# Optimization experiments

Measured on AMD Instinct MI355X. Metric: run time of the kernel, lower is better.

The kernel has to match this reference:

```python
import jax, jax.numpy as jnp
import numpy as np

N_HEADS = 16
WINDOW = 256


def setup_inputs() -> dict:
    key = jax.random.key(0)
    ks = jax.random.split(key, 6)
    B, S, D = 2, 2048, 1024
    std = 0.02
    x = jax.random.normal(ks[0], (B, S, D), dtype=jnp.float32)
    wq = jax.random.normal(ks[1], (D, D), dtype=jnp.float32) * std
    wk = jax.random.normal(ks[2], (D, D), dtype=jnp.float32) * std
    wv = jax.random.normal(ks[3], (D, D), dtype=jnp.float32) * std
    wo = jax.random.normal(ks[4], (D, D), dtype=jnp.float32) * std
    bq = jnp.zeros((D,), jnp.float32)
    bk = jnp.zeros((D,), jnp.float32)
    bv = jnp.zeros((D,), jnp.float32)
    bo = jnp.zeros((D,), jnp.float32)
    return {"x": x, "wq": wq, "bq": bq, "wk": wk, "bk": bk,
            "wv": wv, "bv": bv, "wo": wo, "bo": bo}


def _sliding_window_bias(seq_len: int) -> jnp.ndarray:
    # allowed iff |i - j| <= WINDOW  ->  0.0, else -inf  (matches torch loop mask)
    i = jnp.arange(seq_len)[:, None]
    j = jnp.arange(seq_len)[None, :]
    allowed = jnp.abs(i - j) <= WINDOW
    return jnp.where(allowed, 0.0, -jnp.inf).astype(jnp.float32)


def reference(x, wq, bq, wk, bk, wv, bv, wo, bo):
    B, S, D = x.shape
    H = N_HEADS
    dh = D // H
    scale = dh ** -0.5
    # nn.Linear: y = x @ W^T + b
    q = (x @ wq.T + bq).reshape(B, S, H, dh).transpose(0, 2, 1, 3)  # [B,H,S,dh]
    k = (x @ wk.T + bk).reshape(B, S, H, dh).transpose(0, 2, 1, 3)
    v = (x @ wv.T + bv).reshape(B, S, H, dh).transpose(0, 2, 1, 3)
    scores = jnp.einsum('bhqd,bhkd->bhqk', q, k) * scale  # [B,H,S,S]
    scores = scores + _sliding_window_bias(S)[None, None]
    attn = jax.nn.softmax(scores, axis=-1)
    out = jnp.einsum('bhqk,bhkd->bhqd', attn, v)  # [B,H,S,dh]
    out = out.transpose(0, 2, 1, 3).reshape(B, S, D)
    return out @ wo.T + bo
```

## Files before the change

kernel.cpp:

```cpp
#include <hip/hip_runtime.h>
#include <stdint.h>

static constexpr int Ss = 2048;
static constexpr int Dd = 1024;
static constexpr int Hh = 16;
static constexpr int DH = 64;

typedef short bf16x8 __attribute__((ext_vector_type(8)));
typedef float f32x4 __attribute__((ext_vector_type(4)));

#define LOG2E 1.4426950408889634f

__device__ __forceinline__ uint16_t f2bf(float f) {
  uint32_t u = __builtin_bit_cast(uint32_t, f);
  u += 0x7fffu + ((u >> 16) & 1u);
  return (uint16_t)(u >> 16);
}
__device__ __forceinline__ float bf2f(uint16_t h) {
  uint32_t u = ((uint32_t)h) << 16;
  return __builtin_bit_cast(float, u);
}
__device__ __forceinline__ uint32_t cvtpk(float a, float b) {
  uint32_t r;
  asm("v_cvt_pk_bf16_f32 %0, %1, %2" : "=v"(r) : "v"(a), "v"(b));
  return r;
}

template <int CTRL>
__device__ __forceinline__ float dppf(float x) {
  return __builtin_bit_cast(float,
      __builtin_amdgcn_update_dpp(0, __builtin_bit_cast(int, x), CTRL, 0xF, 0xF, true));
}
__device__ __forceinline__ float rowsum16(float v) {
  v += dppf<0x128>(v);
  v += dppf<0x124>(v);
  v += dppf<0x122>(v);
  v += dppf<0x121>(v);
  return v;
}
__device__ __forceinline__ float fexp2(float x) { return __builtin_amdgcn_exp2f(x); }

#define GAS(p) ((const __attribute__((address_space(1))) uint32_t*)(p))
#define LAS(p) ((__attribute__((address_space(3))) uint32_t*)(p))

__global__ void cvt_all(const float* __restrict__ x,
                        const float* __restrict__ w0, const float* __restrict__ w1,
                        const float* __restrict__ w2, const float* __restrict__ w3,
                        uint16_t* __restrict__ xb,
                        uint16_t* __restrict__ o0, uint16_t* __restrict__ o1,
                        uint16_t* __restrict__ o2, uint16_t* __restrict__ o3) {
  int bid = blockIdx.x;
  const float* in;
  uint16_t* out;
  int i;
  if (bid < 4096) {
    in = x; out = xb; i = bid * 256 + threadIdx.x;
  } else {
    int b2 = bid - 4096;
    int t = b2 >> 10;
    in = (t == 0) ? w0 : (t == 1) ? w1 : (t == 2) ? w2 : w3;
    out = (t == 0) ? o0 : (t == 1) ? o1 : (t == 2) ? o2 : o3;
    i = (b2 & 1023) * 256 + threadIdx.x;
  }
  float4 v = reinterpret_cast<const float4*>(in)[i];
  ushort4 o;
  o.x = f2bf(v.x); o.y = f2bf(v.y); o.z = f2bf(v.z); o.w = f2bf(v.w);
  reinterpret_cast<ushort4*>(out)[i] = o;
}

__global__ __launch_bounds__(256, 2) void gemm_qkv(
    const uint16_t* __restrict__ A,
    const uint16_t* __restrict__ W0, const uint16_t* __restrict__ W1, const uint16_t* __restrict__ W2,
    const float* __restrict__ b0, const float* __restrict__ b1, const float* __restrict__ b2,
    uint16_t* __restrict__ O0, uint16_t* __restrict__ O1, uint16_t* __restrict__ O2) {
  constexpr int K = 1024;
  __shared__ __align__(16) uint8_t ldsA[128 * 128];
  __shared__ __align__(16) uint8_t ldsB[128 * 128];

  const int tid = threadIdx.x, w = tid >> 6, lane = tid & 63;
  const int q = lane & 15, g = lane >> 4;
  const int wm = w >> 1, wn = w & 1;
  const int bx = blockIdx.x, by = blockIdx.y, z = blockIdx.z;
  const uint16_t* Wp = (z == 0) ? W0 : (z == 1) ? W1 : W2;
  const float* bp = (z == 0) ? b0 : (z == 1) ? b1 : b2;
  uint16_t* Op = (z == 0) ? O0 : (z == 1) ? O1 : O2;

  f32x4 acc[4][4] = {};

  const int nkt = K >> 6;
  for (int kt = 0; kt < nkt; ++kt) {
    const int k0 = kt << 6;
    __syncthreads();
#pragma unroll
    for (int i = 0; i < 4; ++i) {
      int Lb = w * 4096 + i * 1024 + lane * 16;
      int row = Lb >> 7, cb = Lb & 127;
      int col = (cb ^ ((row & 7) << 4)) >> 1;
      const uint16_t* srcA = A + (size_t)(bx * 128 + row) * K + k0 + col;
      __builtin_amdgcn_global_load_lds(GAS(srcA), LAS(ldsA + w * 4096 + i * 1024), 16, 0, 0);
      const uint16_t* srcB = Wp + (size_t)(by * 128 + row) * K + k0 + col;
      __builtin_amdgcn_global_load_lds(GAS(srcB), LAS(ldsB + w * 4096 + i * 1024), 16, 0, 0);
    }
    __syncthreads();

    bf16x8 af[4][2], bfg[4][2];
#pragma unroll
    for (int mi = 0; mi < 4; ++mi)
#pragma unroll
      for (int s = 0; s < 2; ++s) {
        int row = wm * 64 + mi * 16 + q;
        int cb = (16 * g + 64 * s) ^ ((row & 7) << 4);
        af[mi][s] = *(const bf16x8*)(ldsA + row * 128 + cb);
      }
#pragma unroll
    for (int ni = 0; ni < 4; ++ni)
#pragma unroll
      for (int s = 0; s < 2; ++s) {
        int row = wn * 64 + ni * 16 + q;
        int cb = (16 * g + 64 * s) ^ ((row & 7) << 4);
        bfg[ni][s] = *(const bf16x8*)(ldsB + row * 128 + cb);
      }
#pragma unroll
    for (int mi = 0; mi < 4; ++mi)
#pragma unroll
      for (int ni = 0; ni < 4; ++ni) {
        acc[mi][ni] = __builtin_amdgcn_mfma_f32_16x16x32_bf16(af[mi][0], bfg[ni][0], acc[mi][ni], 0, 0, 0);
        acc[mi][ni] = __builtin_amdgcn_mfma_f32_16x16x32_bf16(af[mi][1], bfg[ni][1], acc[mi][ni], 0, 0, 0);
      }
  }

  float bias[4];
#pragma unroll
  for (int ni = 0; ni < 4; ++ni) bias[ni] = bp[by * 128 + wn * 64 + ni * 16 + q];
#pragma unroll
  for (int mi = 0; mi < 4; ++mi)
#pragma unroll
    for (int ni = 0; ni < 4; ++ni)
#pragma unroll
      for (int r = 0; r < 4; ++r) {
        int m = bx * 128 + wm * 64 + mi * 16 + 4 * g + r;
        int n = by * 128 + wn * 64 + ni * 16 + q;
        float v = acc[mi][ni][r] + bias[ni];
        int b = m >> 11, s = m & 2047, h = n >> 6, d = n & 63;
        Op[(((size_t)(b * Hh + h) * Ss + s) << 6) + d] = f2bf(v);
      }
}

__global__ __launch_bounds__(256, 2) void gemm_out(
    const uint16_t* __restrict__ A, const uint16_t* __restrict__ W,
    const float* __restrict__ bp, float* __restrict__ O, int M, int N, int K) {
  __shared__ __align__(16) uint8_t ldsA[2][128 * 128];
  __shared__ __align__(16) uint8_t ldsB[2][64 * 128];

  const int tid = threadIdx.x, w = tid >> 6, lane = tid & 63;
  const int q = lane & 15, g = lane >> 4;
  const int wm = w >> 1, wn = w & 1;
  const int bx = blockIdx.x, by = blockIdx.y;

  f32x4 acc[4][2] = {};

  const int Lb4 = lane * 16;
  auto stage = [&](int kt, int buf) {
    const int k0 = kt << 6;
#pragma unroll
    for (int i = 0; i < 4; ++i) {
      int Lb = w * 4096 + i * 1024 + Lb4;
      int row = Lb >> 7, cb = Lb & 127;
      const uint16_t* srcA = A + (size_t)(bx * 128 + row) * K + k0 + ((cb ^ ((row & 7) << 4)) >> 1);
      __builtin_amdgcn_global_load_lds(GAS(srcA), LAS(ldsA[buf] + w * 4096 + i * 1024), 16, 0, 0);
    }
#pragma unroll
    for (int i = 0; i < 2; ++i) {
      int Lb = w * 2048 + i * 1024 + Lb4;
      int row = Lb >> 7, cb = Lb & 127;
      const uint16_t* srcB = W + (size_t)(by * 64 + row) * K + k0 + ((cb ^ ((row & 7) << 4)) >> 1);
      __builtin_amdgcn_global_load_lds(GAS(srcB), LAS(ldsB[buf] + w * 2048 + i * 1024), 16, 0, 0);
    }
  };

  stage(0, 0);

  const int nkt = K >> 6;
  for (int kt = 0; kt < nkt; ++kt) {
    const int cur = kt & 1;
    asm volatile("s_waitcnt vmcnt(0)" ::: "memory");
    __builtin_amdgcn_sched_barrier(0);
    __builtin_amdgcn_s_barrier();
    __builtin_amdgcn_sched_barrier(0);
    if (kt + 1 < nkt) stage(kt + 1, cur ^ 1);

    bf16x8 af[4][2], bfg[2][2];
#pragma unroll
    for (int mi = 0; mi < 4; ++mi)
#pragma unroll
      for (int s = 0; s < 2; ++s) {
        int row = wm * 64 + mi * 16 + q;
        int cb = (16 * g + 64 * s) ^ ((row & 7) << 4);
        af[mi][s] = *(const bf16x8*)(ldsA[cur] + row * 128 + cb);
      }
#pragma unroll
    for (int ni = 0; ni < 2; ++ni)
#pragma unroll
      for (int s = 0; s < 2; ++s) {
        int row = wn * 32 + ni * 16 + q;
        int cb = (16 * g + 64 * s) ^ ((row & 7) << 4);
        bfg[ni][s] = *(const bf16x8*)(ldsB[cur] + row * 128 + cb);
      }
#pragma unroll
    for (int mi = 0; mi < 4; ++mi)
#pragma unroll
      for (int ni = 0; ni < 2; ++ni) {
        acc[mi][ni] = __builtin_amdgcn_mfma_f32_16x16x32_bf16(af[mi][0], bfg[ni][0], acc[mi][ni], 0, 0, 0);
        acc[mi][ni] = __builtin_amdgcn_mfma_f32_16x16x32_bf16(af[mi][1], bfg[ni][1], acc[mi][ni], 0, 0, 0);
      }
  }

  float bias[2];
#pragma unroll
  for (int ni = 0; ni < 2; ++ni) bias[ni] = bp[by * 64 + wn * 32 + ni * 16 + q];
#pragma unroll
  for (int mi = 0; mi < 4; ++mi)
#pragma unroll
    for (int ni = 0; ni < 2; ++ni)
#pragma unroll
      for (int r = 0; r < 4; ++r) {
        int m = bx * 128 + wm * 64 + mi * 16 + 4 * g + r;
        int n = by * 64 + wn * 32 + ni * 16 + q;
        O[(size_t)m * N + n] = acc[mi][ni][r] + bias[ni];
      }
}

__global__ __launch_bounds__(512, 4) void attn_swa(
    const uint16_t* __restrict__ Qg, const uint16_t* __restrict__ Kg,
    const uint16_t* __restrict__ Vg, uint16_t* __restrict__ Og) {
  __shared__ __align__(16) uint8_t ldsK[2][64 * 128];
  __shared__ __align__(16) uint8_t ldsVt[2][64 * 128];
  __shared__ __align__(16) uint8_t ldsP[8][2048];

  const int tid = threadIdx.x, w = tid >> 6, lane = tid & 63;
  const int q = lane & 15, g = lane >> 4;
  const int qb = blockIdx.x, bh = blockIdx.y;
  const size_t hbase = (size_t)bh * Ss * DH;
  const uint16_t* Qp = Qg + hbase;
  const uint16_t* Kp = Kg + hbase;
  const uint16_t* Vp = Vg + hbase;
  const int q0 = qb * 128;
  const int qw = q0 + w * 16;

  bf16x8 aq[2];
#pragma unroll
  for (int s = 0; s < 2; ++s) {
    bf16x8 t = *(const bf16x8*)(Qp + (size_t)(qw + q) * DH + s * 32 + g * 8);
#pragma unroll
    for (int j = 0; j < 8; ++j) {
      float f = bf2f((uint16_t)t[j]) * 0.125f;
      t[j] = (short)f2bf(f);
    }
    aq[s] = t;
  }

  f32x4 accO[4] = {};
  float lrun[4] = {0.f, 0.f, 0.f, 0.f};

  const int t0 = (q0 >= 256) ? (q0 - 256) : 0;
  const int t1 = (q0 + 384 <= Ss) ? (q0 + 384) : Ss;
  const int nt = (t1 - t0) >> 6;

  {
    int Lb = w * 1024 + lane * 16;
    int row = Lb >> 7, cb = Lb & 127;
    const uint16_t* srcK = Kp + (size_t)(t0 + row) * DH + ((cb ^ ((row & 7) << 4)) >> 1);
    __builtin_amdgcn_global_load_lds(GAS(srcK), LAS(ldsK[0] + w * 1024), 16, 0, 0);
  }
  bf16x8 v0 = *(const bf16x8*)(Vp + (size_t)(t0 + lane) * DH + w * 8);

  for (int t = 0; t < nt; ++t) {
    const int kb0 = t0 + (t << 6);
    const int cur = t & 1, nxt = cur ^ 1;

    asm volatile("s_waitcnt vmcnt(0)" ::: "memory");
    uint8_t* Vt = ldsVt[cur];
#pragma unroll
    for (int j = 0; j < 8; ++j) {
      int c = w * 8 + j;
      *(uint16_t*)(Vt + c * 128 + ((2 * lane) ^ (j << 4))) = (uint16_t)v0[j];
    }
    asm volatile("s_waitcnt lgkmcnt(0)" ::: "memory");
    __builtin_amdgcn_sched_barrier(0);
    __builtin_amdgcn_s_barrier();
    __builtin_amdgcn_sched_barrier(0);

    if (t + 1 < nt) {
      int Lb = w * 1024 + lane * 16;
      int row = Lb >> 7, cb = Lb & 127;
      const uint16_t* srcK = Kp + (size_t)(kb0 + 64 + row) * DH + ((cb ^ ((row & 7) << 4)) >> 1);
      __builtin_amdgcn_global_load_lds(GAS(srcK), LAS(ldsK[nxt] + w * 1024), 16, 0, 0);
      v0 = *(const bf16x8*)(Vp + (size_t)(kb0 + 64 + lane) * DH + w * 8);
    }

    const int dtile = kb0 - qw;
    if (dtile >= -319 && dtile <= 271) {
      const uint8_t* Kl = ldsK[cur];
      f32x4 sacc[4] = {};
      __builtin_amdgcn_s_setprio(1);
#pragma unroll
      for (int kb = 0; kb < 4; ++kb) {
        int row = kb * 16 + q;
#pragma unroll
        for (int s = 0; s < 2; ++s) {
          int cb = (16 * g + 64 * s) ^ ((row & 7) << 4);
          bf16x8 bk = *(const bf16x8*)(Kl + row * 128 + cb);
          sacc[kb] = __builtin_amdgcn_mfma_f32_16x16x32_bf16(aq[s], bk, sacc[kb], 0, 0, 0);
        }
      }
      __builtin_amdgcn_s_setprio(0);
      if (dtile < -192 || dtile > 192) {
#pragma unroll
        for (int kb = 0; kb < 4; ++kb) {
          int key = kb0 + kb * 16 + q;
#pragma unroll
          for (int r = 0; r < 4; ++r) {
            int qi = qw + 4 * g + r;
            int dd = qi - key;
            bool ok = (dd <= 256) && (dd >= -256);
            sacc[kb][r] = ok ? sacc[kb][r] : -1e30f;
          }
        }
      }
      uint8_t* Pl = ldsP[w];
#pragma unroll
      for (int r = 0; r < 4; ++r) {
        float p0 = fexp2(sacc[0][r] * LOG2E);
        float p1 = fexp2(sacc[1][r] * LOG2E);
        float p2 = fexp2(sacc[2][r] * LOG2E);
        float p3 = fexp2(sacc[3][r] * LOG2E);
        float rs = rowsum16((p0 + p1) + (p2 + p3));
        lrun[r] += rs;
        int prow = 4 * g + r;
        int sw = (prow & 7) << 4;
        uint8_t* Pr = Pl + prow * 128;
        uint32_t pk01 = cvtpk(p0, p1), pk23 = cvtpk(p2, p3);
        *(uint16_t*)(Pr + ((2 * q) ^ sw))      = (uint16_t)pk01;
        *(uint16_t*)(Pr + ((2 * q + 32) ^ sw)) = (uint16_t)(pk01 >> 16);
        *(uint16_t*)(Pr + ((2 * q + 64) ^ sw)) = (uint16_t)pk23;
        *(uint16_t*)(Pr + ((2 * q + 96) ^ sw)) = (uint16_t)(pk23 >> 16);
      }
      bf16x8 ap[2];
#pragma unroll
      for (int s = 0; s < 2; ++s) {
        int cb = (16 * g + 64 * s) ^ ((q & 7) << 4);
        ap[s] = *(const bf16x8*)(Pl + q * 128 + cb);
      }
      __builtin_amdgcn_s_setprio(1);
#pragma unroll
      for (int db = 0; db < 4; ++db) {
        int vr = db * 16 + q;
#pragma unroll
        for (int s = 0; s < 2; ++s) {
          int cb = (64 * s + 16 * g) ^ ((vr & 7) << 4);
          bf16x8 bvf = *(const bf16x8*)(ldsVt[cur] + vr * 128 + cb);
          accO[db] = __builtin_amdgcn_mfma_f32_16x16x32_bf16(ap[s], bvf, accO[db], 0, 0, 0);
        }
      }
      __builtin_amdgcn_s_setprio(0);
    }
  }

  const int b2 = bh >> 4, h = bh & 15;
#pragma unroll
  for (int r = 0; r < 4; ++r) {
    float inv = 1.0f / lrun[r];
    int qi = qw + 4 * g + r;
    size_t rowbase = ((size_t)(b2 * Ss + qi)) * Dd + h * DH;
#pragma unroll
    for (int db = 0; db < 4; ++db) {
      Og[rowbase + db * 16 + q] = f2bf(accO[db][r] * inv);
    }
  }
}

extern "C" void kernel_launch(void* const* d_in, const int* in_sizes, int n_in,
                              void* d_out, int out_size, void* d_ws, size_t ws_size,
                              hipStream_t stream) {
  const float* x  = (const float*)d_in[0];
  const float* wq = (const float*)d_in[1];
  const float* bq = (const float*)d_in[2];
  const float* wk = (const float*)d_in[3];
  const float* bk = (const float*)d_in[4];
  const float* wv = (const float*)d_in[5];
  const float* bv = (const float*)d_in[6];
  const float* wo = (const float*)d_in[7];
  const float* bo = (const float*)d_in[8];
  float* out = (float*)d_out;

  uint8_t* ws = (uint8_t*)d_ws;
  uint16_t* xb  = (uint16_t*)(ws + (size_t)(0u  << 20));
  uint16_t* wqb = (uint16_t*)(ws + (size_t)(8u  << 20));
  uint16_t* wkb = (uint16_t*)(ws + (size_t)(10u << 20));
  uint16_t* wvb = (uint16_t*)(ws + (size_t)(12u << 20));
  uint16_t* wob = (uint16_t*)(ws + (size_t)(14u << 20));
  uint16_t* Qb  = (uint16_t*)(ws + (size_t)(16u << 20));
  uint16_t* Kb  = (uint16_t*)(ws + (size_t)(24u << 20));
  uint16_t* Vb  = (uint16_t*)(ws + (size_t)(32u << 20));
  uint16_t* AOb = (uint16_t*)(ws + (size_t)(40u << 20));

  cvt_all<<<8192, 256, 0, stream>>>(x, wq, wk, wv, wo, xb, wqb, wkb, wvb, wob);

  gemm_qkv<<<dim3(32, 8, 3), 256, 0, stream>>>(
      xb, wqb, wkb, wvb, bq, bk, bv, Qb, Kb, Vb);

  attn_swa<<<dim3(16, 32), 512, 0, stream>>>(Qb, Kb, Vb, AOb);

  gemm_out<<<dim3(32, 16), 256, 0, stream>>>(
      AOb, wob, bo, out, 4096, 1024, 1024);
}
```

Before: 78.94 us.

## Fuse Q/K/V projections per block and double-buffer LDS loads in QKV GEMM

The QKV GEMM now computes all three projections in one block, so each 128-row tile of x is staged once and reused for Q, K and V, each with a 64-column weight tile. A double-buffered LDS pipeline issues the next k-tile's global-to-LDS loads before computing on the current one, with a single barrier per iteration. The intent is to cut redundant A-tile loads and hide global memory latency behind MFMA work. In exchange LDS use grows to 80KB per block, which may limit occupancy, and the grid shrinks from 768 to 512 blocks.

```diff
diff --git a/kernel.cpp b/kernel.cpp
--- a/kernel.cpp
+++ b/kernel.cpp
@@ -74,76 +74,99 @@
     const float* __restrict__ b0, const float* __restrict__ b1, const float* __restrict__ b2,
     uint16_t* __restrict__ O0, uint16_t* __restrict__ O1, uint16_t* __restrict__ O2) {
   constexpr int K = 1024;
-  __shared__ __align__(16) uint8_t ldsA[128 * 128];
-  __shared__ __align__(16) uint8_t ldsB[128 * 128];
+  __shared__ __align__(16) uint8_t ldsA[2][128 * 128];
+  __shared__ __align__(16) uint8_t ldsB[2][3][64 * 128];
 
   const int tid = threadIdx.x, w = tid >> 6, lane = tid & 63;
   const int q = lane & 15, g = lane >> 4;
   const int wm = w >> 1, wn = w & 1;
-  const int bx = blockIdx.x, by = blockIdx.y, z = blockIdx.z;
-  const uint16_t* Wp = (z == 0) ? W0 : (z == 1) ? W1 : W2;
-  const float* bp = (z == 0) ? b0 : (z == 1) ? b1 : b2;
-  uint16_t* Op = (z == 0) ? O0 : (z == 1) ? O1 : O2;
-
-  f32x4 acc[4][4] = {};
+  const int bx = blockIdx.x, by = blockIdx.y;
+  const uint16_t* Wz[3] = {W0, W1, W2};
+
+  f32x4 acc[3][4][2] = {};
+
+  const int Lb16 = lane * 16;
+  auto stage = [&](int kt, int buf) {
+    const int k0 = kt << 6;
+#pragma unroll
+    for (int i = 0; i < 4; ++i) {
+      int Lb = w * 4096 + i * 1024 + Lb16;
+      int row = Lb >> 7, cb = Lb & 127;
+      const uint16_t* srcA = A + (size_t)(bx * 128 + row) * K + k0 + ((cb ^ ((row & 7) << 4)) >> 1);
+      __builtin_amdgcn_global_load_lds(GAS(srcA), LAS(ldsA[buf] + w * 4096 + i * 1024), 16, 0, 0);
+    }
+#pragma unroll
+    for (int z = 0; z < 3; ++z)
+#pragma unroll
+      for (int i = 0; i < 2; ++i) {
+        int Lb = w * 2048 + i * 1024 + Lb16;
+        int row = Lb >> 7, cb = Lb & 127;
+        const uint16_t* srcB = Wz[z] + (size_t)(by * 64 + row) * K + k0 + ((cb ^ ((row & 7) << 4)) >> 1);
+        __builtin_amdgcn_global_load_lds(GAS(srcB), LAS(ldsB[buf][z] + w * 2048 + i * 1024), 16, 0, 0);
+      }
+  };
+
+  stage(0, 0);
 
   const int nkt = K >> 6;
   for (int kt = 0; kt < nkt; ++kt) {
-    const int k0 = kt << 6;
-    __syncthreads();
-#pragma unroll
-    for (int i = 0; i < 4; ++i) {
-      int Lb = w * 4096 + i * 1024 + lane * 16;
-      int row = Lb >> 7, cb = Lb & 127;
-      int col = (cb ^ ((row & 7) << 4)) >> 1;
-      const uint16_t* srcA = A + (size_t)(bx * 128 + row) * K + k0 + col;
-      __builtin_amdgcn_global_load_lds(GAS(srcA), LAS(ldsA + w * 4096 + i * 1024), 16, 0, 0);
-      const uint16_t* srcB = Wp + (size_t)(by * 128 + row) * K + k0 + col;
-      __builtin_amdgcn_global_load_lds(GAS(srcB), LAS(ldsB + w * 4096 + i * 1024), 16, 0, 0);
-    }
-    __syncthreads();
-
-    bf16x8 af[4][2], bfg[4][2];
+    const int cur = kt & 1;
+    asm volatile("s_waitcnt vmcnt(0)" ::: "memory");
+    __builtin_amdgcn_sched_barrier(0);
+    __builtin_amdgcn_s_barrier();
+    __builtin_amdgcn_sched_barrier(0);
+    if (kt + 1 < nkt) stage(kt + 1, cur ^ 1);
+
+    bf16x8 af[4][2];
 #pragma unroll
     for (int mi = 0; mi < 4; ++mi)
 #pragma unroll
       for (int s = 0; s < 2; ++s) {
         int row = wm * 64 + mi * 16 + q;
         int cb = (16 * g + 64 * s) ^ ((row & 7) << 4);
-        af[mi][s] = *(const bf16x8*)(ldsA + row * 128 + cb);
-      }
-#pragma unroll
-    for (int ni = 0; ni < 4; ++ni)
-#pragma unroll
-      for (int s = 0; s < 2; ++s) {
-        int row = wn * 64 + ni * 16 + q;
-        int cb = (16 * g + 64 * s) ^ ((row & 7) << 4);
-        bfg[ni][s] = *(const bf16x8*)(ldsB + row * 128 + cb);
-      }
+        af[mi][s] = *(const bf16x8*)(ldsA[cur] + row * 128 + cb);
+      }
+#pragma unroll
+    for (int z = 0; z < 3; ++z) {
+      bf16x8 bfg[2][2];
+#pragma unroll
+      for (int ni = 0; ni < 2; ++ni)
+#pragma unroll
+        for (int s = 0; s < 2; ++s) {
+          int row = wn * 32 + ni * 16 + q;
+          int cb = (16 * g + 64 * s) ^ ((row & 7) << 4);
+          bfg[ni][s] = *(const bf16x8*)(ldsB[cur][z] + row * 128 + cb);
+        }
+#pragma unroll
+      for (int mi = 0; mi < 4; ++mi)
+#pragma unroll
+        for (int ni = 0; ni < 2; ++ni) {
+          acc[z][mi][ni] = __builtin_amdgcn_mfma_f32_16x16x32_bf16(af[mi][0], bfg[ni][0], acc[z][mi][ni], 0, 0, 0);
+          acc[z][mi][ni] = __builtin_amdgcn_mfma_f32_16x16x32_bf16(af[mi][1], bfg[ni][1], acc[z][mi][ni], 0, 0, 0);
+        }
+    }
+  }
+
+  const float* bz[3] = {b0, b1, b2};
+  uint16_t* Oz[3] = {O0, O1, O2};
+#pragma unroll
+  for (int z = 0; z < 3; ++z) {
+    float bias[2];
+#pragma unroll
+    for (int ni = 0; ni < 2; ++ni) bias[ni] = bz[z][by * 64 + wn * 32 + ni * 16 + q];
 #pragma unroll
     for (int mi = 0; mi < 4; ++mi)
 #pragma unroll
-      for (int ni = 0; ni < 4; ++ni) {
-        acc[mi][ni] = __builtin_amdgcn_mfma_f32_16x16x32_bf16(af[mi][0], bfg[ni][0], acc[mi][ni], 0, 0, 0);
-        acc[mi][ni] = __builtin_amdgcn_mfma_f32_16x16x32_bf16(af[mi][1], bfg[ni][1], acc[mi][ni], 0, 0, 0);
-      }
-  }
-
-  float bias[4];
-#pragma unroll
-  for (int ni = 0; ni < 4; ++ni) bias[ni] = bp[by * 128 + wn * 64 + ni * 16 + q];
-#pragma unroll
-  for (int mi = 0; mi < 4; ++mi)
-#pragma unroll
-    for (int ni = 0; ni < 4; ++ni)
-#pragma unroll
-      for (int r = 0; r < 4; ++r) {
-        int m = bx * 128 + wm * 64 + mi * 16 + 4 * g + r;
-        int n = by * 128 + wn * 64 + ni * 16 + q;
-        float v = acc[mi][ni][r] + bias[ni];
-        int b = m >> 11, s = m & 2047, h = n >> 6, d = n & 63;
-        Op[(((size_t)(b * Hh + h) * Ss + s) << 6) + d] = f2bf(v);
-      }
+      for (int ni = 0; ni < 2; ++ni)
+#pragma unroll
+        for (int r = 0; r < 4; ++r) {
+          int m = bx * 128 + wm * 64 + mi * 16 + 4 * g + r;
+          int n = by * 64 + wn * 32 + ni * 16 + q;
+          float v = acc[z][mi][ni][r] + bias[ni];
+          int b = m >> 11, s = m & 2047, h = n >> 6, d = n & 63;
+          Oz[z][(((size_t)(b * Hh + h) * Ss + s) << 6) + d] = f2bf(v);
+        }
+  }
 }
 
 __global__ __launch_bounds__(256, 2) void gemm_out(
@@ -406,7 +429,7 @@
 
   cvt_all<<<8192, 256, 0, stream>>>(x, wq, wk, wv, wo, xb, wqb, wkb, wvb, wob);
 
-  gemm_qkv<<<dim3(32, 8, 3), 256, 0, stream>>>(
+  gemm_qkv<<<dim3(32, 16), 256, 0, stream>>>(
       xb, wqb, wkb, wvb, bq, bk, bv, Qb, Kb, Vb);
 
   attn_swa<<<dim3(16, 32), 512, 0, stream>>>(Qb, Kb, Vb, AOb);
```

Result: no change. 78.31 us (median of 2 runs) (-0.8%).
